# Kernel tuning notes

Measured on AMD Instinct MI355X. Metric: run time of the kernel, lower is better.

## Reference

```python
import jax, jax.numpy as jnp
import numpy as np

D = 128
N = 262144

def setup_inputs() -> dict:
    key = jax.random.key(0)
    ks = jax.random.split(key, 10)
    inp = {
        'member_embeddings': 0.1 * jax.random.normal(ks[0], (N, D), dtype=jnp.float32),
        'item_embedding': 0.1 * jax.random.normal(ks[1], (D,), dtype=jnp.float32),
        # nn.Linear params (torch convention: y = x @ W.T + b)
        'W_c1': jax.random.normal(ks[2], (D, D), dtype=jnp.float32) / np.sqrt(D),
        'b_c1': jnp.zeros((D,), dtype=jnp.float32),
        'W_c2': jax.random.normal(ks[3], (D, D), dtype=jnp.float32) / np.sqrt(D),
        'b_c2': jnp.zeros((D,), dtype=jnp.float32),
        'w_pa': jax.random.normal(ks[4], (D,), dtype=jnp.float32) / np.sqrt(D),  # peer_attention weight (1,D) squeezed
        'b_pa': jnp.zeros((), dtype=jnp.float32),
        'w_vc': jax.random.normal(ks[5], (D,), dtype=jnp.float32) / np.sqrt(D),  # v_c weight (1,D) squeezed
        'b_vc': jnp.zeros((), dtype=jnp.float32),
    }
    return inp

def reference(member_embeddings, item_embedding, W_c1, b_c1, W_c2, b_c2, w_pa, b_pa, w_vc, b_vc):
    E = member_embeddings  # [N, D]
    # SP: self persistence scores  alpha_SP_i = u_i^T v
    sp = E @ item_embedding  # [N]
    # Peer scores are per-member scalars shared across all exclusion sets.
    s = E @ w_pa + b_pa                       # [N]
    m = jnp.max(s)
    e = jnp.exp(s - m)                        # [N]
    S = jnp.sum(e)                            # scalar
    eE = e[:, None] * E                       # [N, D]
    sum_eE = jnp.sum(eE, axis=0)              # [D]
    # softmax over peers excluding i (exact: softmax is shift-invariant)
    denom = S - e                             # [N]
    peer_agg = (sum_eE[None, :] - eE) / denom[:, None]  # [N, D]
    # PI: v_c^T ReLU(W_c1 u_i + W_c2 peer_agg_i + b)
    h = E @ W_c1.T + b_c1 + peer_agg @ W_c2.T + b_c2     # [N, D]
    pi = jax.nn.relu(h) @ w_vc + b_vc                    # [N]  (dropout = identity in eval)
    alpha = jnp.float32(1.0)
    beta = jnp.float32(1.0)
    attention_weights = jax.nn.softmax(alpha * sp + beta * pi, axis=0)  # [N]
    group_embedding = attention_weights @ E               # [D]
    return (group_embedding, attention_weights)
```

## Files before the change

kernel.cpp:

```cpp
#include <hip/hip_runtime.h>
#include <hip/hip_bf16.h>

#define DIM 128

typedef __attribute__((ext_vector_type(8))) short bf16x8;
typedef __attribute__((ext_vector_type(4))) float f32x4;

#define WS_B12    0
#define WS_C      128
#define WS_SUMEE  256
#define WS_S      384
#define WS_ZB     416
#define WS_GEB    512
#define WS_WBF    4608
#define WS_EEP    20992
#define WS_SEP    152064
#define WS_SP     153088
#define WS_E      415232
#define WS_WEXP   677376
#define WS_EBF    939520

__device__ __forceinline__ unsigned short f2bf(float f) {
    union { float f; unsigned u; } v; v.f = f;
    unsigned r = v.u + 0x7fffu + ((v.u >> 16) & 1u);
    return (unsigned short)(r >> 16);
}

__device__ __forceinline__ float bfbits(unsigned u) {
    union { unsigned u; float f; } v; v.u = u;
    return v.f;
}

__device__ __forceinline__ unsigned pkbf(float a, float b) {
    union { __hip_bfloat162 h; unsigned u; } cv;
    cv.h = __float22bfloat162_rn(make_float2(a, b));
    return cv.u;
}

__global__ __launch_bounds__(256) void k2_stats(const float* __restrict__ E,
                                                const float* __restrict__ v,
                                                const float* __restrict__ wpa,
                                                const float* __restrict__ bpa,
                                                const float* __restrict__ Wc1,
                                                const float* __restrict__ Wc2,
                                                const float* __restrict__ bc1,
                                                const float* __restrict__ bc2,
                                                float* __restrict__ ws) {
    __shared__ float red[16][128];
    __shared__ float redS[16];
    int t = threadIdx.x;

    int gid = blockIdx.x * 256 + t;
    unsigned short* wbf_w = (unsigned short*)(ws + WS_WBF);
    if (gid < 32768) {
        int n = gid >> 7, k = gid & 127;
        float val = (n < 128) ? Wc1[n * 128 + k] : Wc2[(n - 128) * 128 + k];
        wbf_w[gid] = f2bf(val);
    }
    if (gid < 4096) ws[WS_GEB + gid] = 0.f;
    if (gid < 128) ws[WS_B12 + gid] = bc1[gid] + bc2[gid];
    if (gid < 64) ws[WS_ZB + gid] = 0.f;

    int wave = t >> 6, lane = t & 63;
    int cl = lane & 15, rs = lane >> 4;
    int row0 = blockIdx.x * 256;
    const float4* E4 = (const float4*)E;
    unsigned short* ebf = (unsigned short*)(ws + WS_EBF);

    float4 va = ((const float4*)v)[cl];
    float4 vb = ((const float4*)v)[16 + cl];
    float4 pa = ((const float4*)wpa)[cl];
    float4 pb = ((const float4*)wpa)[16 + cl];
    float bias = bpa[0];

    float4 acc0 = {0.f, 0.f, 0.f, 0.f}, acc1 = {0.f, 0.f, 0.f, 0.f};
    float se = 0.f;
    float* sp_ws = ws + WS_SP;
    float* e_ws = ws + WS_E;

#pragma unroll 4
    for (int it = 0; it < 16; ++it) {
        int row = row0 + it * 16 + wave * 4 + rs;
        float4 x0 = E4[row * 32 + cl];
        float4 x1 = E4[row * 32 + 16 + cl];
        unsigned p0 = pkbf(x0.x, x0.y);
        unsigned p1 = pkbf(x0.z, x0.w);
        unsigned p2 = pkbf(x1.x, x1.y);
        unsigned p3 = pkbf(x1.z, x1.w);
        *(uint2*)(ebf + (size_t)row * 128 + cl * 4) = make_uint2(p0, p1);
        *(uint2*)(ebf + (size_t)row * 128 + 64 + cl * 4) = make_uint2(p2, p3);

        float dv = x0.x * va.x + x0.y * va.y + x0.z * va.z + x0.w * va.w
                 + x1.x * vb.x + x1.y * vb.y + x1.z * vb.z + x1.w * vb.w;
        float dp = x0.x * pa.x + x0.y * pa.y + x0.z * pa.z + x0.w * pa.w
                 + x1.x * pb.x + x1.y * pb.y + x1.z * pb.z + x1.w * pb.w;
        for (int off = 1; off < 16; off <<= 1) {
            dv += __shfl_xor(dv, off);
            dp += __shfl_xor(dp, off);
        }
        float e = __expf(dp + bias);
        if (cl == 0) {
            sp_ws[row] = dv;
            e_ws[row] = e;
            se += e;
        }
        acc0.x += e * x0.x; acc0.y += e * x0.y; acc0.z += e * x0.z; acc0.w += e * x0.w;
        acc1.x += e * x1.x; acc1.y += e * x1.y; acc1.z += e * x1.z; acc1.w += e * x1.w;
    }
    int rr = wave * 4 + rs;
    float* dst = red[rr];
    dst[cl * 4 + 0] = acc0.x; dst[cl * 4 + 1] = acc0.y;
    dst[cl * 4 + 2] = acc0.z; dst[cl * 4 + 3] = acc0.w;
    dst[64 + cl * 4 + 0] = acc1.x; dst[64 + cl * 4 + 1] = acc1.y;
    dst[64 + cl * 4 + 2] = acc1.z; dst[64 + cl * 4 + 3] = acc1.w;
    if (cl == 0) redS[rr] = se;
    __syncthreads();
    if (t < 128) {
        float s = 0.f;
#pragma unroll
        for (int r = 0; r < 16; ++r) s += red[r][t];
        ws[WS_EEP + t * 1024 + blockIdx.x] = s;
    }
    if (t == 0) {
        float s = 0.f;
#pragma unroll
        for (int r = 0; r < 16; ++r) s += redS[r];
        ws[WS_SEP + blockIdx.x] = s;
    }
}

__global__ __launch_bounds__(256) void k2b_reduce(float* __restrict__ ws) {
    __shared__ float r4[4];
    int t = threadIdx.x, blk = blockIdx.x;
    const float* src = (blk < 128) ? (ws + WS_EEP + blk * 1024) : (ws + WS_SEP);
    float s = src[t] + src[t + 256] + src[t + 512] + src[t + 768];
    for (int off = 1; off < 64; off <<= 1) s += __shfl_xor(s, off);
    if ((t & 63) == 0) r4[t >> 6] = s;
    __syncthreads();
    if (t == 0) {
        float tot = r4[0] + r4[1] + r4[2] + r4[3];
        if (blk < 128) ws[WS_SUMEE + blk] = tot;
        else ws[WS_S] = tot;
    }
}

__global__ __launch_bounds__(512, 4) void k4_main(const float* __restrict__ wvc,
                                                  const float* __restrict__ bvc_p,
                                                  const float* __restrict__ Wc2,
                                                  float* __restrict__ ws) {
    __shared__ unsigned short Elds[2][64 * 136];
    __shared__ __align__(16) float aux[1032];
    float* pim_a  = aux;
    float* e_l    = aux + 512;
    float* di_l   = aux + 640;
    float* c_lds  = aux + 768;
    float* gep_a  = aux;
    float* zw     = aux + 1024;

    int t = threadIdx.x;
    int w = t >> 6, lane = t & 63, cl = lane & 15, q = lane >> 4;
    int blk = blockIdx.x;
    int row_base = blk * 256;
    const unsigned short* wbf = (const unsigned short*)(ws + WS_WBF);
    const unsigned short* EbBase = (const unsigned short*)(ws + WS_EBF);

    float bvc = bvc_p[0];
    float Sv = ws[WS_S];
    int r0 = w * 8 + q * 2;

    bf16x8 aw1[4], aw2[4];
#pragma unroll
    for (int kt = 0; kt < 4; ++kt) {
        aw1[kt] = *(const bf16x8*)(wbf + (w * 16 + cl) * 128 + kt * 32 + q * 8);
        aw2[kt] = *(const bf16x8*)(wbf + (128 + w * 16 + cl) * 128 + kt * 32 + q * 8);
    }

    float b12r[4], wvr[4];
#pragma unroll
    for (int reg = 0; reg < 4; ++reg) {
        int jr = w * 16 + q * 4 + reg;
        b12r[reg] = ws[WS_B12 + jr];
        wvr[reg] = wvc[jr];
    }

    if (t < 128) {
        const float4* row = (const float4*)(Wc2 + t * 128);
        const float4* se4 = (const float4*)(ws + WS_SUMEE);
        float4 s4 = {0.f, 0.f, 0.f, 0.f};
#pragma unroll
        for (int k = 0; k < 32; ++k) {
            float4 a = row[k], b = se4[k];
            s4.x += a.x * b.x; s4.y += a.y * b.y; s4.z += a.z * b.z; s4.w += a.w * b.w;
        }
        c_lds[t] = s4.x + s4.y + s4.z + s4.w;
    }

    {
        const unsigned short* Eb0 = EbBase + (size_t)row_base * 128;
        uint4 s0 = *(const uint4*)(Eb0 + t * 8);
        uint4 s1 = *(const uint4*)(Eb0 + (t + 512) * 8);
        int r = t >> 4, c = t & 15;
        *(uint4*)&Elds[0][r * 136 + c * 8] = s0;
        int t1 = t + 512; r = t1 >> 4; c = t1 & 15;
        *(uint4*)&Elds[0][r * 136 + c * 8] = s1;
    }
    if (t < 64) {
        float ev = ws[WS_E + row_base + t];
        e_l[t] = ev;
        di_l[t] = 1.0f / (Sv - ev);
    }
    __syncthreads();

    float cjr[4];
#pragma unroll
    for (int reg = 0; reg < 4; ++reg) cjr[reg] = c_lds[w * 16 + q * 4 + reg];

    float z_lane = 0.f;
    float acc8[8] = {0.f, 0.f, 0.f, 0.f, 0.f, 0.f, 0.f, 0.f};

    for (int it = 0; it < 4; ++it) {
        int cur = it & 1, nxt = cur ^ 1;
        int trow0 = row_base + it * 64;
        bool has_next = (it < 3);

        uint4 s0, s1;
        float evN = 0.f;
        if (has_next) {
            const unsigned short* EbN = EbBase + (size_t)(trow0 + 64) * 128;
            s0 = *(const uint4*)(EbN + t * 8);
            s1 = *(const uint4*)(EbN + (t + 512) * 8);
            if (t < 64) evN = ws[WS_E + trow0 + 64 + t];
        }
        float sp0 = ws[WS_SP + trow0 + r0];
        float sp1 = ws[WS_SP + trow0 + r0 + 1];

        f32x4 acc[4][2];
#pragma unroll
        for (int rt = 0; rt < 4; ++rt) {
            acc[rt][0] = (f32x4){0.f, 0.f, 0.f, 0.f};
            acc[rt][1] = (f32x4){0.f, 0.f, 0.f, 0.f};
        }
#pragma unroll
        for (int rt = 0; rt < 4; ++rt) {
            bf16x8 b[4];
#pragma unroll
            for (int kt = 0; kt < 4; ++kt)
                b[kt] = *(const bf16x8*)&Elds[cur][(rt * 16 + cl) * 136 + kt * 32 + q * 8];
#pragma unroll
            for (int kt = 0; kt < 4; ++kt) {
                acc[rt][0] = __builtin_amdgcn_mfma_f32_16x16x32_bf16(aw1[kt], b[kt], acc[rt][0], 0, 0, 0);
                acc[rt][1] = __builtin_amdgcn_mfma_f32_16x16x32_bf16(aw2[kt], b[kt], acc[rt][1], 0, 0, 0);
            }
        }

#pragma unroll
        for (int rt = 0; rt < 4; ++rt) {
            float e_v = e_l[cur * 64 + rt * 16 + cl];
            float di_v = di_l[cur * 64 + rt * 16 + cl];
            float p = 0.f;
#pragma unroll
            for (int reg = 0; reg < 4; ++reg) {
                float h = acc[rt][0][reg] + b12r[reg] + (cjr[reg] - e_v * acc[rt][1][reg]) * di_v;
                p = fmaf(wvr[reg], fmaxf(h, 0.f), p);
            }
            p += __shfl_xor(p, 16);
            p += __shfl_xor(p, 32);
            if (lane < 16) pim_a[w * 64 + rt * 16 + lane] = p;
        }
        __syncthreads();

        float pi0 = 0.f, pi1 = 0.f;
#pragma unroll
        for (int wv = 0; wv < 8; ++wv) {
            pi0 += pim_a[wv * 64 + r0];
            pi1 += pim_a[wv * 64 + r0 + 1];
        }
        float we0 = __expf(sp0 + bvc + pi0);
        float we1 = __expf(sp1 + bvc + pi1);
        if (cl == 0) {
            ws[WS_WEXP + trow0 + r0] = we0;
            ws[WS_WEXP + trow0 + r0 + 1] = we1;
        }
        z_lane += we0 + we1;

#pragma unroll
        for (int rr = 0; rr < 2; ++rr) {
            int r = r0 + rr;
            float wer = rr ? we1 : we0;
            uint4 u = *(const uint4*)&Elds[cur][r * 136 + cl * 8];
            acc8[0] += wer * bfbits(u.x << 16);
            acc8[1] += wer * bfbits(u.x & 0xffff0000u);
            acc8[2] += wer * bfbits(u.y << 16);
            acc8[3] += wer * bfbits(u.y & 0xffff0000u);
            acc8[4] += wer * bfbits(u.z << 16);
            acc8[5] += wer * bfbits(u.z & 0xffff0000u);
            acc8[6] += wer * bfbits(u.w << 16);
            acc8[7] += wer * bfbits(u.w & 0xffff0000u);
        }

        if (has_next) {
            int r = t >> 4, c = t & 15;
            *(uint4*)&Elds[nxt][r * 136 + c * 8] = s0;
            int t1 = t + 512; r = t1 >> 4; c = t1 & 15;
            *(uint4*)&Elds[nxt][r * 136 + c * 8] = s1;
            if (t < 64) {
                e_l[nxt * 64 + t] = evN;
                di_l[nxt * 64 + t] = 1.0f / (Sv - evN);
            }
        }
        __syncthreads();
    }

    z_lane += __shfl_xor(z_lane, 16);
    z_lane += __shfl_xor(z_lane, 32);
    if (lane == 0) zw[w] = z_lane;

#pragma unroll
    for (int jj = 0; jj < 8; ++jj) {
        acc8[jj] += __shfl_xor(acc8[jj], 16);
        acc8[jj] += __shfl_xor(acc8[jj], 32);
    }
    if (lane < 16) {
        *(float4*)&gep_a[w * 128 + cl * 8] = (float4){acc8[0], acc8[1], acc8[2], acc8[3]};
        *(float4*)&gep_a[w * 128 + cl * 8 + 4] = (float4){acc8[4], acc8[5], acc8[6], acc8[7]};
    }
    __syncthreads();

    if (t < 128) {
        float tot = 0.f;
#pragma unroll
        for (int wv = 0; wv < 8; ++wv) tot += gep_a[wv * 128 + t];
        atomicAdd(&ws[WS_GEB + (blk & 31) * 128 + t], tot);
    }
    if (t == 128) {
        float zs = zw[0] + zw[1] + zw[2] + zw[3] + zw[4] + zw[5] + zw[6] + zw[7];
        atomicAdd(&ws[WS_ZB + (blk & 63)], zs);
    }
}

__global__ __launch_bounds__(256) void k5_final(const float* __restrict__ ws,
                                                float* __restrict__ out) {
    int t = threadIdx.x, blk = blockIdx.x;
    float z = ws[WS_ZB + (t & 63)];
    for (int off = 1; off < 64; off <<= 1) z += __shfl_xor(z, off);
    float invZ = 1.0f / z;
    if (blk < 1024) {
        int i = blk * 256 + t;
        out[128 + i] = ws[WS_WEXP + i] * invZ;
    } else if (t < 128) {
        float s = 0.f;
#pragma unroll
        for (int b = 0; b < 32; ++b) s += ws[WS_GEB + b * 128 + t];
        out[t] = s * invZ;
    }
}

extern "C" void kernel_launch(void* const* d_in, const int* in_sizes, int n_in,
                              void* d_out, int out_size, void* d_ws, size_t ws_size,
                              hipStream_t stream) {
    const float* E   = (const float*)d_in[0];
    const float* v   = (const float*)d_in[1];
    const float* Wc1 = (const float*)d_in[2];
    const float* bc1 = (const float*)d_in[3];
    const float* Wc2 = (const float*)d_in[4];
    const float* bc2 = (const float*)d_in[5];
    const float* wpa = (const float*)d_in[6];
    const float* bpa = (const float*)d_in[7];
    const float* wvc = (const float*)d_in[8];
    const float* bvc = (const float*)d_in[9];
    float* ws  = (float*)d_ws;
    float* out = (float*)d_out;

    k2_stats<<<1024, 256, 0, stream>>>(E, v, wpa, bpa, Wc1, Wc2, bc1, bc2, ws);
    k2b_reduce<<<129, 256, 0, stream>>>(ws);
    k4_main<<<1024, 512, 0, stream>>>(wvc, bvc, Wc2, ws);
    k5_final<<<1025, 256, 0, stream>>>(ws, out);
}
```

Measured before the change: 274.1 us.

## Triple-buffer E tiles in k4_main to drop one barrier per iteration

Moves the main k4 loop from a double-buffered E tile in LDS to a triple-buffered one, prefetching two tiles ahead in registers. Each iteration now has a single __syncthreads instead of two. The per-wave partial pi values are double-buffered and stored transposed, so each thread reads them back as float4 vectors, and e and 1/(S-e) are packed together into float2 pairs. The cost is more LDS per block (a third 17 KB buffer), which may lower occupancy, and more registers held live for the prefetch.

```diff
diff --git a/kernel.cpp b/kernel.cpp
--- a/kernel.cpp
+++ b/kernel.cpp
@@ -148,14 +148,13 @@
                                                   const float* __restrict__ bvc_p,
                                                   const float* __restrict__ Wc2,
                                                   float* __restrict__ ws) {
-    __shared__ unsigned short Elds[2][64 * 136];
-    __shared__ __align__(16) float aux[1032];
-    float* pim_a  = aux;
-    float* e_l    = aux + 512;
-    float* di_l   = aux + 640;
-    float* c_lds  = aux + 768;
-    float* gep_a  = aux;
-    float* zw     = aux + 1024;
+    __shared__ unsigned short Elds[3][64 * 136];
+    __shared__ __align__(16) float arena[1544];
+    float* pim2  = arena;
+    float* ed    = arena + 1024;
+    float* c_lds = arena + 1408;
+    float* zw    = arena + 1536;
+    float* gep_a = arena;
 
     int t = threadIdx.x;
     int w = t >> 6, lane = t & 63, cl = lane & 15, q = lane >> 4;
@@ -167,6 +166,8 @@
     float bvc = bvc_p[0];
     float Sv = ws[WS_S];
     int r0 = w * 8 + q * 2;
+    int sr = t >> 4, sc = t & 15;
+    int sr1 = (t + 512) >> 4, sc1 = (t + 512) & 15;
 
     bf16x8 aw1[4], aw2[4];
 #pragma unroll
@@ -197,17 +198,22 @@
 
     {
         const unsigned short* Eb0 = EbBase + (size_t)row_base * 128;
-        uint4 s0 = *(const uint4*)(Eb0 + t * 8);
-        uint4 s1 = *(const uint4*)(Eb0 + (t + 512) * 8);
-        int r = t >> 4, c = t & 15;
-        *(uint4*)&Elds[0][r * 136 + c * 8] = s0;
-        int t1 = t + 512; r = t1 >> 4; c = t1 & 15;
-        *(uint4*)&Elds[0][r * 136 + c * 8] = s1;
+        uint4 a0 = *(const uint4*)(Eb0 + t * 8);
+        uint4 a1 = *(const uint4*)(Eb0 + (t + 512) * 8);
+        *(uint4*)&Elds[0][sr * 136 + sc * 8] = a0;
+        *(uint4*)&Elds[0][sr1 * 136 + sc1 * 8] = a1;
     }
     if (t < 64) {
         float ev = ws[WS_E + row_base + t];
-        e_l[t] = ev;
-        di_l[t] = 1.0f / (Sv - ev);
+        *(float2*)&ed[t * 2] = make_float2(ev, 1.0f / (Sv - ev));
+    }
+    uint4 sN0, sN1;
+    float evN = 0.f;
+    {
+        const unsigned short* Eb1 = EbBase + (size_t)(row_base + 64) * 128;
+        sN0 = *(const uint4*)(Eb1 + t * 8);
+        sN1 = *(const uint4*)(Eb1 + (t + 512) * 8);
+        if (t < 64) evN = ws[WS_E + row_base + 64 + t];
     }
     __syncthreads();
 
@@ -219,17 +225,21 @@
     float acc8[8] = {0.f, 0.f, 0.f, 0.f, 0.f, 0.f, 0.f, 0.f};
 
     for (int it = 0; it < 4; ++it) {
-        int cur = it & 1, nxt = cur ^ 1;
+        int cur = it % 3;
+        int pb = it & 1;
         int trow0 = row_base + it * 64;
-        bool has_next = (it < 3);
-
-        uint4 s0, s1;
-        float evN = 0.f;
-        if (has_next) {
-            const unsigned short* EbN = EbBase + (size_t)(trow0 + 64) * 128;
-            s0 = *(const uint4*)(EbN + t * 8);
-            s1 = *(const uint4*)(EbN + (t + 512) * 8);
-            if (t < 64) evN = ws[WS_E + trow0 + 64 + t];
+
+        if (it < 3) {
+            int wr = (it + 1) % 3;
+            *(uint4*)&Elds[wr][sr * 136 + sc * 8] = sN0;
+            *(uint4*)&Elds[wr][sr1 * 136 + sc1 * 8] = sN1;
+            if (t < 64) *(float2*)&ed[(wr * 64 + t) * 2] = make_float2(evN, 1.0f / (Sv - evN));
+        }
+        if (it < 2) {
+            const unsigned short* EbN = EbBase + (size_t)(trow0 + 128) * 128;
+            sN0 = *(const uint4*)(EbN + t * 8);
+            sN1 = *(const uint4*)(EbN + (t + 512) * 8);
+            if (t < 64) evN = ws[WS_E + trow0 + 128 + t];
         }
         float sp0 = ws[WS_SP + trow0 + r0];
         float sp1 = ws[WS_SP + trow0 + r0 + 1];
@@ -255,26 +265,23 @@
 
 #pragma unroll
         for (int rt = 0; rt < 4; ++rt) {
-            float e_v = e_l[cur * 64 + rt * 16 + cl];
-            float di_v = di_l[cur * 64 + rt * 16 + cl];
+            float2 edv = *(const float2*)&ed[(cur * 64 + rt * 16 + cl) * 2];
             float p = 0.f;
 #pragma unroll
             for (int reg = 0; reg < 4; ++reg) {
-                float h = acc[rt][0][reg] + b12r[reg] + (cjr[reg] - e_v * acc[rt][1][reg]) * di_v;
+                float h = acc[rt][0][reg] + b12r[reg] + (cjr[reg] - edv.x * acc[rt][1][reg]) * edv.y;
                 p = fmaf(wvr[reg], fmaxf(h, 0.f), p);
             }
             p += __shfl_xor(p, 16);
             p += __shfl_xor(p, 32);
-            if (lane < 16) pim_a[w * 64 + rt * 16 + lane] = p;
+            if (lane < 16) pim2[(pb * 64 + rt * 16 + lane) * 8 + w] = p;
         }
         __syncthreads();
 
-        float pi0 = 0.f, pi1 = 0.f;
-#pragma unroll
-        for (int wv = 0; wv < 8; ++wv) {
-            pi0 += pim_a[wv * 64 + r0];
-            pi1 += pim_a[wv * 64 + r0 + 1];
-        }
+        const float4* pr = (const float4*)&pim2[(pb * 64 + r0) * 8];
+        float4 Pa = pr[0], Pb = pr[1], Pc = pr[2], Pd = pr[3];
+        float pi0 = (Pa.x + Pa.y + Pa.z + Pa.w) + (Pb.x + Pb.y + Pb.z + Pb.w);
+        float pi1 = (Pc.x + Pc.y + Pc.z + Pc.w) + (Pd.x + Pd.y + Pd.z + Pd.w);
         float we0 = __expf(sp0 + bvc + pi0);
         float we1 = __expf(sp1 + bvc + pi1);
         if (cl == 0) {
@@ -297,19 +304,9 @@
             acc8[6] += wer * bfbits(u.w << 16);
             acc8[7] += wer * bfbits(u.w & 0xffff0000u);
         }
-
-        if (has_next) {
-            int r = t >> 4, c = t & 15;
-            *(uint4*)&Elds[nxt][r * 136 + c * 8] = s0;
-            int t1 = t + 512; r = t1 >> 4; c = t1 & 15;
-            *(uint4*)&Elds[nxt][r * 136 + c * 8] = s1;
-            if (t < 64) {
-                e_l[nxt * 64 + t] = evN;
-                di_l[nxt * 64 + t] = 1.0f / (Sv - evN);
-            }
-        }
-        __syncthreads();
-    }
+    }
+
+    __syncthreads();
 
     z_lane += __shfl_xor(z_lane, 16);
     z_lane += __shfl_xor(z_lane, 32);
```

Result: faster. 264.5 us (-3.5%).
